# Kernel tuning notes

Hardware: AMD Instinct MI355X
Metric: run time of the kernel (lower is better)

The kernel has to match this reference:

```python
import jax, jax.numpy as jnp
import numpy as np

TEMPERATURE = 0.04
LAMBDA_KOLEO = 0.1
EPS_NORM = 1e-12
EPS_KOLEO = 1e-9


def setup_inputs() -> dict:
    key = jax.random.key(0)
    k1, k2 = jax.random.split(key)
    N, D = 8192, 512
    z1 = jax.random.normal(k1, (N, D), dtype=jnp.float32)
    z2 = jax.random.normal(k2, (N, D), dtype=jnp.float32)
    return {"z1": z1, "z2": z2}


def _l2_normalize(x):
    # matches F.normalize(x, dim=1) with default eps=1e-12
    n = jnp.linalg.norm(x, axis=1, keepdims=True)
    return x / jnp.maximum(n, EPS_NORM)


def _infonce(queries, keys, temperature):
    # [N, N] similarity logits; labels are the diagonal
    logits = (queries @ keys.T) / temperature
    logp = jax.nn.log_softmax(logits, axis=1)
    return -jnp.mean(jnp.diagonal(logp))


def _koleo(emb):
    # pairwise euclidean distances via gram trick (matches torch.cdist p=2)
    sq = jnp.sum(emb * emb, axis=1)
    d2 = sq[:, None] + sq[None, :] - 2.0 * (emb @ emb.T)
    d = jnp.sqrt(jnp.maximum(d2, 0.0))
    N = emb.shape[0]
    eye = jnp.eye(N, dtype=bool)
    d = jnp.where(eye, jnp.inf, d)
    min_d = jnp.min(d, axis=1)
    return -jnp.mean(jnp.log(min_d + EPS_KOLEO))


def reference(z1, z2):
    z1 = _l2_normalize(z1)
    z2 = _l2_normalize(z2)
    loss_12 = _infonce(z1, z2, TEMPERATURE)
    loss_21 = _infonce(z2, z1, TEMPERATURE)
    loss_contrastive = (loss_12 + loss_21) / 2
    koleo_1 = _koleo(z1)
    koleo_2 = _koleo(z2)
    loss_koleo = (koleo_1 + koleo_2) / 2
    total_loss = loss_contrastive + LAMBDA_KOLEO * loss_koleo
    return total_loss
```

## Files before the change

kernel.cpp:

```cpp
#include <hip/hip_runtime.h>
#include <hip/hip_bf16.h>
#include <hip/hip_fp8.h>
#include <math.h>

#define N 8192
#define D 512
#define BM 128
#define BK 64
#define NSTRIP 64
#define S_BLOCKS (NSTRIP * NSTRIP)
#define TRI (NSTRIP * (NSTRIP + 1) / 2)
#define G_BLOCKS (2 * TRI)
#define SG_BLOCKS (S_BLOCKS + G_BLOCKS)

typedef float f32x16 __attribute__((ext_vector_type(16)));
typedef int i32x4 __attribute__((ext_vector_type(4)));
typedef int i32x8 __attribute__((ext_vector_type(8)));

__device__ inline void gload_lds16(const void* g, void* l) {
  __builtin_amdgcn_global_load_lds(
      (const __attribute__((address_space(1))) void*)g,
      (__attribute__((address_space(3))) void*)l, 16, 0, 0);
}

__global__ __launch_bounds__(256) void norm_kernel(
    const float* __restrict__ z1, const float* __restrict__ z2,
    unsigned char* __restrict__ q1, unsigned char* __restrict__ q2,
    float* __restrict__ diag, float* __restrict__ out) {
  int row = blockIdx.x;
  int t = threadIdx.x;
  if (row == 0 && t == 0) out[0] = 0.0f;
  const float* a = z1 + (size_t)row * D;
  const float* b = z2 + (size_t)row * D;
  float va[2], vb[2];
  float ss1 = 0.f, ss2 = 0.f, dd = 0.f;
#pragma unroll
  for (int i = 0; i < 2; i++) {
    float x = a[t + 256 * i];
    float y = b[t + 256 * i];
    va[i] = x; vb[i] = y;
    ss1 += x * x; ss2 += y * y; dd += x * y;
  }
#pragma unroll
  for (int off = 1; off < 64; off <<= 1) {
    ss1 += __shfl_xor(ss1, off);
    ss2 += __shfl_xor(ss2, off);
    dd  += __shfl_xor(dd,  off);
  }
  __shared__ float red[3][4];
  int wv = t >> 6;
  if ((t & 63) == 0) { red[0][wv] = ss1; red[1][wv] = ss2; red[2][wv] = dd; }
  __syncthreads();
  ss1 = red[0][0] + red[0][1] + red[0][2] + red[0][3];
  ss2 = red[1][0] + red[1][1] + red[1][2] + red[1][3];
  dd  = red[2][0] + red[2][1] + red[2][2] + red[2][3];
  float i1 = 1.0f / fmaxf(sqrtf(ss1), 1e-12f);
  float i2 = 1.0f / fmaxf(sqrtf(ss2), 1e-12f);
#pragma unroll
  for (int i = 0; i < 2; i++) {
    __hip_fp8_e4m3 c1((float)(va[i] * i1));
    __hip_fp8_e4m3 c2((float)(vb[i] * i2));
    q1[(size_t)row * D + t + 256 * i] = c1.__x;
    q2[(size_t)row * D + t + 256 * i] = c2.__x;
  }
  if (t == 0) diag[row] = dd * i1 * i2;
}

__device__ __forceinline__ void stage_tile(
    const unsigned char* __restrict__ P, int base, int k0,
    unsigned char* T, int t) {
#pragma unroll
  for (int it = 0; it < 2; it++) {
    int s = it * 256 + t;
    int row = s >> 2, cs = s & 3;
    int src = cs ^ ((row >> 1) & 3);
    gload_lds16(P + (size_t)(base + row) * D + k0 + src * 16, &T[s * 16]);
  }
}

__device__ __forceinline__ void mm_tile_mx(
    const unsigned char* __restrict__ X, const unsigned char* __restrict__ Y,
    int r0, int c0, unsigned char* At0, unsigned char* Bt0,
    unsigned char* At1, unsigned char* Bt1, f32x16 (&acc)[2][2],
    int t, int l31, int kl, int rw, int cw) {
#pragma unroll
  for (int i = 0; i < 2; i++)
#pragma unroll
    for (int j = 0; j < 2; j++)
#pragma unroll
      for (int r = 0; r < 16; r++) acc[i][j][r] = 0.0f;

  int offA[2][2], offB[2][2];
#pragma unroll
  for (int i = 0; i < 2; i++) {
    int row = rw * 64 + i * 32 + l31;
    int sw = (row >> 1) & 3;
    offA[i][0] = row * 64 + (((kl << 1) | 0) ^ sw) * 16;
    offA[i][1] = row * 64 + (((kl << 1) | 1) ^ sw) * 16;
  }
#pragma unroll
  for (int j = 0; j < 2; j++) {
    int row = cw * 64 + j * 32 + l31;
    int sw = (row >> 1) & 3;
    offB[j][0] = row * 64 + (((kl << 1) | 0) ^ sw) * 16;
    offB[j][1] = row * 64 + (((kl << 1) | 1) ^ sw) * 16;
  }

  stage_tile(X, r0, 0, At0, t);
  stage_tile(Y, c0, 0, Bt0, t);

#pragma unroll 2
  for (int kc = 0; kc < 8; kc++) {
    unsigned char* Ac = (kc & 1) ? At1 : At0;
    unsigned char* Bc = (kc & 1) ? Bt1 : Bt0;
    unsigned char* An = (kc & 1) ? At0 : At1;
    unsigned char* Bn = (kc & 1) ? Bt0 : Bt1;
    __syncthreads();
    if (kc < 7) {
      stage_tile(X, r0, (kc + 1) * BK, An, t);
      stage_tile(Y, c0, (kc + 1) * BK, Bn, t);
    }
    i32x8 af[2], bf[2];
#pragma unroll
    for (int i = 0; i < 2; i++) {
      i32x4 lo = *(const i32x4*)&Ac[offA[i][0]];
      i32x4 hi = *(const i32x4*)&Ac[offA[i][1]];
      af[i] = __builtin_shufflevector(lo, hi, 0, 1, 2, 3, 4, 5, 6, 7);
    }
#pragma unroll
    for (int j = 0; j < 2; j++) {
      i32x4 lo = *(const i32x4*)&Bc[offB[j][0]];
      i32x4 hi = *(const i32x4*)&Bc[offB[j][1]];
      bf[j] = __builtin_shufflevector(lo, hi, 0, 1, 2, 3, 4, 5, 6, 7);
    }
#pragma unroll
    for (int i = 0; i < 2; i++)
#pragma unroll
      for (int j = 0; j < 2; j++)
        acc[i][j] = __builtin_amdgcn_mfma_scale_f32_32x32x64_f8f6f4(
            af[i], bf[j], acc[i][j], 0 , 0 ,
            0, 0x7F7F7F7F, 0, 0x7F7F7F7F);
  }
}

__global__ __launch_bounds__(256, 3) void sg_kernel(
    const unsigned char* __restrict__ q1, const unsigned char* __restrict__ q2,
    float* __restrict__ rowS, float* __restrict__ colS,
    float* __restrict__ partG) {
  __shared__ unsigned char At0[BM * BK];
  __shared__ unsigned char Bt0[BM * BK];
  __shared__ unsigned char At1[BM * BK];
  __shared__ unsigned char Bt1[BM * BK];
  __shared__ float redA[2][BM];
  __shared__ float redB[2][BM];

  int bxr = blockIdx.x;
  int bx = (bxr & 7) * (SG_BLOCKS / 8) + (bxr >> 3);

  int t = threadIdx.x;
  int lane = t & 63;
  int wave = t >> 6;
  int l31 = lane & 31;
  int h = lane >> 5;
  int rw = wave >> 1;
  int cw = wave & 1;
  const float scale = 1.4426950408889634f / 0.04f;

  bool smode = bx < S_BLOCKS;
  const unsigned char* X;
  const unsigned char* Y;
  int r0, c0, ga = 0, gb = 0, gg = 0;
  bool diagb = false;
  if (smode) {
    r0 = (bx >> 6) * BM;
    c0 = (bx & 63) * BM;
    X = q1; Y = q2;
  } else {
    int gx = bx - S_BLOCKS;
    gg = (gx >= TRI) ? 1 : 0;
    int tri = gx - gg * TRI;
    int a = (int)((sqrtf(8.0f * (float)tri + 1.0f) - 1.0f) * 0.5f);
    while ((a + 1) * (a + 2) / 2 <= tri) a++;
    while (a * (a + 1) / 2 > tri) a--;
    int b = tri - a * (a + 1) / 2;
    ga = a; gb = b;
    X = gg ? q2 : q1; Y = X;
    r0 = a * BM;
    c0 = b * BM;
    diagb = (a == b);
  }

  f32x16 acc[2][2];
  mm_tile_mx(X, Y, r0, c0, At0, Bt0, At1, Bt1, acc, t, l31, h, rw, cw);

  if (smode) {
    float csum[2] = {0.0f, 0.0f};
#pragma unroll
    for (int i = 0; i < 2; i++) {
      float rsum[16];
#pragma unroll
      for (int reg = 0; reg < 16; reg++) rsum[reg] = 0.0f;
#pragma unroll
      for (int j = 0; j < 2; j++)
#pragma unroll
        for (int reg = 0; reg < 16; reg++) {
          float e = __builtin_amdgcn_exp2f(acc[i][j][reg] * scale);
          rsum[reg] += e;
          csum[j] += e;
        }
#pragma unroll
      for (int reg = 0; reg < 16; reg++) {
#pragma unroll
        for (int off = 1; off < 32; off <<= 1) rsum[reg] += __shfl_xor(rsum[reg], off);
      }
      if (l31 == 0) {
#pragma unroll
        for (int reg = 0; reg < 16; reg++) {
          int rloc = (reg & 3) + 8 * (reg >> 2) + 4 * h;
          redB[cw][rw * 64 + i * 32 + rloc] = rsum[reg];
        }
      }
    }
#pragma unroll
    for (int j = 0; j < 2; j++) {
      csum[j] += __shfl_xor(csum[j], 32);
      if (h == 0) redA[rw][cw * 64 + j * 32 + l31] = csum[j];
    }
    __syncthreads();
    if (t < BM) {
      colS[(size_t)(r0 >> 7) * N + c0 + t] = redA[0][t] + redA[1][t];
      rowS[(size_t)(c0 >> 7) * N + r0 + t] = redB[0][t] + redB[1][t];
    }
  } else {
#pragma unroll
    for (int i = 0; i < 2; i++) {
      float rmax[16];
#pragma unroll
      for (int reg = 0; reg < 16; reg++) {
        int rloc = (reg & 3) + 8 * (reg >> 2) + 4 * h;
        int rr = rw * 64 + i * 32 + rloc;
        float v = -3.0e38f;
#pragma unroll
        for (int j = 0; j < 2; j++) {
          float x = acc[i][j][reg];
          int cc = cw * 64 + j * 32 + l31;
          if (diagb && cc == rr) x = -3.0e38f;
          v = fmaxf(v, x);
        }
        rmax[reg] = v;
      }
#pragma unroll
      for (int reg = 0; reg < 16; reg++) {
#pragma unroll
        for (int off = 1; off < 32; off <<= 1) rmax[reg] = fmaxf(rmax[reg], __shfl_xor(rmax[reg], off));
      }
      if (l31 == 0) {
#pragma unroll
        for (int reg = 0; reg < 16; reg++) {
          int rloc = (reg & 3) + 8 * (reg >> 2) + 4 * h;
          redA[cw][rw * 64 + i * 32 + rloc] = rmax[reg];
        }
      }
    }
    if (!diagb) {
#pragma unroll
      for (int j = 0; j < 2; j++) {
        float m = -3.0e38f;
#pragma unroll
        for (int i = 0; i < 2; i++)
#pragma unroll
          for (int reg = 0; reg < 16; reg++) m = fmaxf(m, acc[i][j][reg]);
        m = fmaxf(m, __shfl_xor(m, 32));
        if (h == 0) redB[rw][cw * 64 + j * 32 + l31] = m;
      }
    }
    __syncthreads();
    if (t < BM) {
      partG[((size_t)(gg * NSTRIP + gb)) * N + r0 + t] = fmaxf(redA[0][t], redA[1][t]);
      if (!diagb)
        partG[((size_t)(gg * NSTRIP + ga)) * N + c0 + t] = fmaxf(redB[0][t], redB[1][t]);
    }
  }
}

__global__ __launch_bounds__(256) void combine_kernel(
    const float* __restrict__ diag,
    const float* __restrict__ rowS, const float* __restrict__ colS,
    const float* __restrict__ partG, float* __restrict__ out) {
  const float invT = 25.0f;
  int i = blockIdx.x * 256 + threadIdx.x;

  float s = 0.0f;
  for (int q = 0; q < NSTRIP; q++) s += rowS[(size_t)q * N + i];
  float a12 = logf(s) - diag[i] * invT;

  s = 0.0f;
  for (int o = 0; o < NSTRIP; o++) s += colS[(size_t)o * N + i];
  float a21 = logf(s) - diag[i] * invT;

  float g1 = -3.0e38f, g2 = -3.0e38f;
  for (int o = 0; o < NSTRIP; o++) {
    g1 = fmaxf(g1, partG[(size_t)o * N + i]);
    g2 = fmaxf(g2, partG[(size_t)(NSTRIP + o) * N + i]);
  }
  float k1 = logf(sqrtf(fmaxf(2.0f - 2.0f * g1, 0.0f)) + 1e-9f);
  float k2 = logf(sqrtf(fmaxf(2.0f - 2.0f * g2, 0.0f)) + 1e-9f);

  float c = 0.5f * (a12 + a21) / (float)N - 0.1f * 0.5f * (k1 + k2) / (float)N;
#pragma unroll
  for (int off = 1; off < 64; off <<= 1) c += __shfl_xor(c, off);
  __shared__ float fr[4];
  int wv = threadIdx.x >> 6;
  if ((threadIdx.x & 63) == 0) fr[wv] = c;
  __syncthreads();
  if (threadIdx.x == 0)
    atomicAdd(out, fr[0] + fr[1] + fr[2] + fr[3]);
}

extern "C" void kernel_launch(void* const* d_in, const int* in_sizes, int n_in,
                              void* d_out, int out_size, void* d_ws, size_t ws_size,
                              hipStream_t stream) {
  const float* z1 = (const float*)d_in[0];
  const float* z2 = (const float*)d_in[1];
  char* w = (char*)d_ws;
  unsigned char* q1 = (unsigned char*)w; w += (size_t)N * D;
  unsigned char* q2 = (unsigned char*)w; w += (size_t)N * D;
  float* diag = (float*)w;   w += (size_t)N * sizeof(float);
  float* rowS = (float*)w;   w += (size_t)NSTRIP * N * sizeof(float);
  float* colS = (float*)w;   w += (size_t)NSTRIP * N * sizeof(float);
  float* partG = (float*)w;  w += (size_t)2 * NSTRIP * N * sizeof(float);
  float* out = (float*)d_out;

  norm_kernel<<<N, 256, 0, stream>>>(z1, z2, q1, q2, diag, out);
  sg_kernel<<<SG_BLOCKS, 256, 0, stream>>>(q1, q2, rowS, colS, partG);
  combine_kernel<<<N / 256, 256, 0, stream>>>(diag, rowS, colS, partG, out);
}
```

Before: 216.4 us.

## Deepen LDS pipeline to four buffers, vectorize norm, and parallelize combine

The GEMM tile loop now keeps four LDS buffers, loading two K-chunks ahead, and issues eight MFMAs per barrier with raised wave priority. Launch bounds drop from 3 to 2 blocks per CU to make room for the larger LDS footprint, and the reduction scratch reuses the tile buffers. The XCD-aware block index remapping is removed. The norm kernel uses float2 loads and uchar2 stores, and the combine kernel splits the 64-strip reduction across four waves, using 128 blocks instead of 32. The aim is fewer barriers and more load/compute overlap, at the cost of occupancy and L2 locality.

```diff
diff --git a/kernel.cpp b/kernel.cpp
--- a/kernel.cpp
+++ b/kernel.cpp
@@ -30,17 +30,13 @@
   int row = blockIdx.x;
   int t = threadIdx.x;
   if (row == 0 && t == 0) out[0] = 0.0f;
-  const float* a = z1 + (size_t)row * D;
-  const float* b = z2 + (size_t)row * D;
-  float va[2], vb[2];
-  float ss1 = 0.f, ss2 = 0.f, dd = 0.f;
-#pragma unroll
-  for (int i = 0; i < 2; i++) {
-    float x = a[t + 256 * i];
-    float y = b[t + 256 * i];
-    va[i] = x; vb[i] = y;
-    ss1 += x * x; ss2 += y * y; dd += x * y;
-  }
+  const float2* a = (const float2*)(z1 + (size_t)row * D);
+  const float2* b = (const float2*)(z2 + (size_t)row * D);
+  float2 xa = a[t];
+  float2 xb = b[t];
+  float ss1 = xa.x * xa.x + xa.y * xa.y;
+  float ss2 = xb.x * xb.x + xb.y * xb.y;
+  float dd = xa.x * xb.x + xa.y * xb.y;
 #pragma unroll
   for (int off = 1; off < 64; off <<= 1) {
     ss1 += __shfl_xor(ss1, off);
@@ -56,107 +52,120 @@
   dd  = red[2][0] + red[2][1] + red[2][2] + red[2][3];
   float i1 = 1.0f / fmaxf(sqrtf(ss1), 1e-12f);
   float i2 = 1.0f / fmaxf(sqrtf(ss2), 1e-12f);
-#pragma unroll
-  for (int i = 0; i < 2; i++) {
-    __hip_fp8_e4m3 c1((float)(va[i] * i1));
-    __hip_fp8_e4m3 c2((float)(vb[i] * i2));
-    q1[(size_t)row * D + t + 256 * i] = c1.__x;
-    q2[(size_t)row * D + t + 256 * i] = c2.__x;
-  }
+  __hip_fp8_e4m3 c1a(xa.x * i1), c1b(xa.y * i1);
+  __hip_fp8_e4m3 c2a(xb.x * i2), c2b(xb.y * i2);
+  uchar2 u1; u1.x = c1a.__x; u1.y = c1b.__x;
+  uchar2 u2; u2.x = c2a.__x; u2.y = c2b.__x;
+  ((uchar2*)q1)[(size_t)row * 256 + t] = u1;
+  ((uchar2*)q2)[(size_t)row * 256 + t] = u2;
   if (t == 0) diag[row] = dd * i1 * i2;
 }
 
-__device__ __forceinline__ void stage_tile(
-    const unsigned char* __restrict__ P, int base, int k0,
-    unsigned char* T, int t) {
-#pragma unroll
-  for (int it = 0; it < 2; it++) {
-    int s = it * 256 + t;
-    int row = s >> 2, cs = s & 3;
-    int src = cs ^ ((row >> 1) & 3);
-    gload_lds16(P + (size_t)(base + row) * D + k0 + src * 16, &T[s * 16]);
-  }
+__device__ __forceinline__ void stage_pair(
+    const unsigned char* pA, const unsigned char* pB,
+    unsigned char (*Ab)[BM * BK], unsigned char (*Bb)[BM * BK],
+    int ldst, int chunk) {
+  int buf = chunk & 3;
+  int k0 = chunk * BK;
+  gload_lds16(pA + k0, &Ab[buf][ldst]);
+  gload_lds16(pA + 64 * D + k0, &Ab[buf][4096 + ldst]);
+  gload_lds16(pB + k0, &Bb[buf][ldst]);
+  gload_lds16(pB + 64 * D + k0, &Bb[buf][4096 + ldst]);
 }
 
 __device__ __forceinline__ void mm_tile_mx(
     const unsigned char* __restrict__ X, const unsigned char* __restrict__ Y,
-    int r0, int c0, unsigned char* At0, unsigned char* Bt0,
-    unsigned char* At1, unsigned char* Bt1, f32x16 (&acc)[2][2],
-    int t, int l31, int kl, int rw, int cw) {
+    int r0, int c0, unsigned char (*Ab)[BM * BK], unsigned char (*Bb)[BM * BK],
+    f32x16 (&acc)[2][2], int t, int l31, int h, int rw, int cw) {
 #pragma unroll
   for (int i = 0; i < 2; i++)
 #pragma unroll
     for (int j = 0; j < 2; j++)
 #pragma unroll
       for (int r = 0; r < 16; r++) acc[i][j][r] = 0.0f;
+
+  int srow = t >> 2;
+  int ssrc = (t & 3) ^ ((t >> 3) & 3);
+  const unsigned char* pA = X + (size_t)(r0 + srow) * D + ssrc * 16;
+  const unsigned char* pB = Y + (size_t)(c0 + srow) * D + ssrc * 16;
+  int ldst = t * 16;
 
   int offA[2][2], offB[2][2];
 #pragma unroll
   for (int i = 0; i < 2; i++) {
     int row = rw * 64 + i * 32 + l31;
     int sw = (row >> 1) & 3;
-    offA[i][0] = row * 64 + (((kl << 1) | 0) ^ sw) * 16;
-    offA[i][1] = row * 64 + (((kl << 1) | 1) ^ sw) * 16;
+    offA[i][0] = row * 64 + (((h << 1) | 0) ^ sw) * 16;
+    offA[i][1] = row * 64 + (((h << 1) | 1) ^ sw) * 16;
   }
 #pragma unroll
   for (int j = 0; j < 2; j++) {
     int row = cw * 64 + j * 32 + l31;
     int sw = (row >> 1) & 3;
-    offB[j][0] = row * 64 + (((kl << 1) | 0) ^ sw) * 16;
-    offB[j][1] = row * 64 + (((kl << 1) | 1) ^ sw) * 16;
-  }
-
-  stage_tile(X, r0, 0, At0, t);
-  stage_tile(Y, c0, 0, Bt0, t);
-
-#pragma unroll 2
-  for (int kc = 0; kc < 8; kc++) {
-    unsigned char* Ac = (kc & 1) ? At1 : At0;
-    unsigned char* Bc = (kc & 1) ? Bt1 : Bt0;
-    unsigned char* An = (kc & 1) ? At0 : At1;
-    unsigned char* Bn = (kc & 1) ? Bt0 : Bt1;
+    offB[j][0] = row * 64 + (((h << 1) | 0) ^ sw) * 16;
+    offB[j][1] = row * 64 + (((h << 1) | 1) ^ sw) * 16;
+  }
+
+  stage_pair(pA, pB, Ab, Bb, ldst, 0);
+  stage_pair(pA, pB, Ab, Bb, ldst, 1);
+
+#pragma unroll
+  for (int p = 0; p < 4; p++) {
     __syncthreads();
-    if (kc < 7) {
-      stage_tile(X, r0, (kc + 1) * BK, An, t);
-      stage_tile(Y, c0, (kc + 1) * BK, Bn, t);
-    }
-    i32x8 af[2], bf[2];
+    if (p < 3) {
+      stage_pair(pA, pB, Ab, Bb, ldst, 2 * p + 2);
+      stage_pair(pA, pB, Ab, Bb, ldst, 2 * p + 3);
+    }
+    const unsigned char* A0 = Ab[(2 * p) & 3];
+    const unsigned char* B0 = Bb[(2 * p) & 3];
+    const unsigned char* A1 = Ab[(2 * p + 1) & 3];
+    const unsigned char* B1 = Bb[(2 * p + 1) & 3];
+    i32x8 a0[2], b0[2], a1[2], b1[2];
 #pragma unroll
     for (int i = 0; i < 2; i++) {
-      i32x4 lo = *(const i32x4*)&Ac[offA[i][0]];
-      i32x4 hi = *(const i32x4*)&Ac[offA[i][1]];
-      af[i] = __builtin_shufflevector(lo, hi, 0, 1, 2, 3, 4, 5, 6, 7);
+      i32x4 lo = *(const i32x4*)(A0 + offA[i][0]);
+      i32x4 hi = *(const i32x4*)(A0 + offA[i][1]);
+      a0[i] = __builtin_shufflevector(lo, hi, 0, 1, 2, 3, 4, 5, 6, 7);
+      lo = *(const i32x4*)(A1 + offA[i][0]);
+      hi = *(const i32x4*)(A1 + offA[i][1]);
+      a1[i] = __builtin_shufflevector(lo, hi, 0, 1, 2, 3, 4, 5, 6, 7);
     }
 #pragma unroll
     for (int j = 0; j < 2; j++) {
-      i32x4 lo = *(const i32x4*)&Bc[offB[j][0]];
-      i32x4 hi = *(const i32x4*)&Bc[offB[j][1]];
-      bf[j] = __builtin_shufflevector(lo, hi, 0, 1, 2, 3, 4, 5, 6, 7);
-    }
+      i32x4 lo = *(const i32x4*)(B0 + offB[j][0]);
+      i32x4 hi = *(const i32x4*)(B0 + offB[j][1]);
+      b0[j] = __builtin_shufflevector(lo, hi, 0, 1, 2, 3, 4, 5, 6, 7);
+      lo = *(const i32x4*)(B1 + offB[j][0]);
+      hi = *(const i32x4*)(B1 + offB[j][1]);
+      b1[j] = __builtin_shufflevector(lo, hi, 0, 1, 2, 3, 4, 5, 6, 7);
+    }
+    __builtin_amdgcn_s_setprio(1);
 #pragma unroll
     for (int i = 0; i < 2; i++)
 #pragma unroll
       for (int j = 0; j < 2; j++)
         acc[i][j] = __builtin_amdgcn_mfma_scale_f32_32x32x64_f8f6f4(
-            af[i], bf[j], acc[i][j], 0 , 0 ,
-            0, 0x7F7F7F7F, 0, 0x7F7F7F7F);
-  }
-}
-
-__global__ __launch_bounds__(256, 3) void sg_kernel(
+            a0[i], b0[j], acc[i][j], 0, 0, 0, 0x7F7F7F7F, 0, 0x7F7F7F7F);
+#pragma unroll
+    for (int i = 0; i < 2; i++)
+#pragma unroll
+      for (int j = 0; j < 2; j++)
+        acc[i][j] = __builtin_amdgcn_mfma_scale_f32_32x32x64_f8f6f4(
+            a1[i], b1[j], acc[i][j], 0, 0, 0, 0x7F7F7F7F, 0, 0x7F7F7F7F);
+    __builtin_amdgcn_s_setprio(0);
+  }
+}
+
+__global__ __launch_bounds__(256, 2) void sg_kernel(
     const unsigned char* __restrict__ q1, const unsigned char* __restrict__ q2,
     float* __restrict__ rowS, float* __restrict__ colS,
     float* __restrict__ partG) {
-  __shared__ unsigned char At0[BM * BK];
-  __shared__ unsigned char Bt0[BM * BK];
-  __shared__ unsigned char At1[BM * BK];
-  __shared__ unsigned char Bt1[BM * BK];
-  __shared__ float redA[2][BM];
-  __shared__ float redB[2][BM];
-
-  int bxr = blockIdx.x;
-  int bx = (bxr & 7) * (SG_BLOCKS / 8) + (bxr >> 3);
-
+  __shared__ unsigned char Ab[4][BM * BK];
+  __shared__ unsigned char Bb[4][BM * BK];
+  float (*redA)[BM] = reinterpret_cast<float (*)[BM]>(&Ab[0][0]);
+  float (*redB)[BM] = reinterpret_cast<float (*)[BM]>(&Ab[0][0] + 1024);
+
+  int bx = blockIdx.x;
   int t = threadIdx.x;
   int lane = t & 63;
   int wave = t >> 6;
@@ -191,7 +200,9 @@
   }
 
   f32x16 acc[2][2];
-  mm_tile_mx(X, Y, r0, c0, At0, Bt0, At1, Bt1, acc, t, l31, h, rw, cw);
+  mm_tile_mx(X, Y, r0, c0, Ab, Bb, acc, t, l31, h, rw, cw);
+
+  __syncthreads();
 
   if (smode) {
     float csum[2] = {0.0f, 0.0f};
@@ -287,34 +298,38 @@
     const float* __restrict__ diag,
     const float* __restrict__ rowS, const float* __restrict__ colS,
     const float* __restrict__ partG, float* __restrict__ out) {
-  const float invT = 25.0f;
-  int i = blockIdx.x * 256 + threadIdx.x;
-
-  float s = 0.0f;
-  for (int q = 0; q < NSTRIP; q++) s += rowS[(size_t)q * N + i];
-  float a12 = logf(s) - diag[i] * invT;
-
-  s = 0.0f;
-  for (int o = 0; o < NSTRIP; o++) s += colS[(size_t)o * N + i];
-  float a21 = logf(s) - diag[i] * invT;
-
-  float g1 = -3.0e38f, g2 = -3.0e38f;
-  for (int o = 0; o < NSTRIP; o++) {
-    g1 = fmaxf(g1, partG[(size_t)o * N + i]);
-    g2 = fmaxf(g2, partG[(size_t)(NSTRIP + o) * N + i]);
-  }
-  float k1 = logf(sqrtf(fmaxf(2.0f - 2.0f * g1, 0.0f)) + 1e-9f);
-  float k2 = logf(sqrtf(fmaxf(2.0f - 2.0f * g2, 0.0f)) + 1e-9f);
-
-  float c = 0.5f * (a12 + a21) / (float)N - 0.1f * 0.5f * (k1 + k2) / (float)N;
-#pragma unroll
-  for (int off = 1; off < 64; off <<= 1) c += __shfl_xor(c, off);
-  __shared__ float fr[4];
-  int wv = threadIdx.x >> 6;
-  if ((threadIdx.x & 63) == 0) fr[wv] = c;
+  int t = threadIdx.x;
+  int l = t & 63;
+  int w = t >> 6;
+  int i = blockIdx.x * 64 + l;
+
+  float sR = 0.0f, sC = 0.0f, g1 = -3.0e38f, g2 = -3.0e38f;
+#pragma unroll
+  for (int s = 0; s < 16; s++) {
+    int strip = w * 16 + s;
+    sR += rowS[(size_t)strip * N + i];
+    sC += colS[(size_t)strip * N + i];
+    g1 = fmaxf(g1, partG[(size_t)strip * N + i]);
+    g2 = fmaxf(g2, partG[(size_t)(NSTRIP + strip) * N + i]);
+  }
+  __shared__ float red[4][4][64];
+  red[0][w][l] = sR; red[1][w][l] = sC; red[2][w][l] = g1; red[3][w][l] = g2;
   __syncthreads();
-  if (threadIdx.x == 0)
-    atomicAdd(out, fr[0] + fr[1] + fr[2] + fr[3]);
+  if (w == 0) {
+    sR = red[0][0][l] + red[0][1][l] + red[0][2][l] + red[0][3][l];
+    sC = red[1][0][l] + red[1][1][l] + red[1][2][l] + red[1][3][l];
+    g1 = fmaxf(fmaxf(red[2][0][l], red[2][1][l]), fmaxf(red[2][2][l], red[2][3][l]));
+    g2 = fmaxf(fmaxf(red[3][0][l], red[3][1][l]), fmaxf(red[3][2][l], red[3][3][l]));
+    float dv = diag[i] * 25.0f;
+    float a12 = logf(sR) - dv;
+    float a21 = logf(sC) - dv;
+    float k1 = logf(sqrtf(fmaxf(2.0f - 2.0f * g1, 0.0f)) + 1e-9f);
+    float k2 = logf(sqrtf(fmaxf(2.0f - 2.0f * g2, 0.0f)) + 1e-9f);
+    float c = 0.5f * (a12 + a21) / (float)N - 0.1f * 0.5f * (k1 + k2) / (float)N;
+#pragma unroll
+    for (int off = 1; off < 64; off <<= 1) c += __shfl_xor(c, off);
+    if (l == 0) atomicAdd(out, c);
+  }
 }
 
 extern "C" void kernel_launch(void* const* d_in, const int* in_sizes, int n_in,
@@ -333,5 +348,5 @@
 
   norm_kernel<<<N, 256, 0, stream>>>(z1, z2, q1, q2, diag, out);
   sg_kernel<<<SG_BLOCKS, 256, 0, stream>>>(q1, q2, rowS, colS, partG);
-  combine_kernel<<<N / 256, 256, 0, stream>>>(diag, rowS, colS, partG, out);
-}
+  combine_kernel<<<N / 64, 256, 0, stream>>>(diag, rowS, colS, partG, out);
+}
```

New measurement: 238.5 us. 10.2% more time.
